# Performance work log

Hardware: AMD Instinct MI355X
Metric: run time of the kernel (lower is better)

Reference implementation:

```python
import jax, jax.numpy as jnp
import numpy as np

B, S, HID = 1, 2048, 2048
HQ, HKV, D = 16, 4, 128
BS = 64            # seerattn gate block size
GH = 128           # gate hidden size
INTER = 5632
THR = 0.004        # seerattn_threshold on softmaxed block gate scores
EPS = 1e-6
NEG = -1e30


def _rms(x, w):
    xf = x.astype(jnp.float32)
    var = jnp.mean(xf * xf, axis=-1, keepdims=True)
    return (w * (xf * jax.lax.rsqrt(var + EPS))).astype(x.dtype)


def _rotate_half(x):
    x1, x2 = jnp.split(x, 2, axis=-1)
    return jnp.concatenate([-x2, x1], axis=-1)


def setup_inputs() -> dict:
    key = jax.random.key(0)
    ks = jax.random.split(key, 16)
    s = 0.02
    pos = jnp.arange(S, dtype=jnp.float32)
    inv_freq = 1.0 / (1e6 ** (jnp.arange(0, D, 2, dtype=jnp.float32) / D))
    freqs = pos[:, None] * inv_freq[None, :]
    emb = jnp.concatenate([freqs, freqs], axis=-1)  # [S, D]
    return {
        'hidden_states': jax.random.normal(ks[0], (B, S, HID), jnp.float32),
        'cos': jnp.cos(emb),
        'sin': jnp.sin(emb),
        'ln1_w': jnp.ones((HID,), jnp.float32),
        'ln2_w': jnp.ones((HID,), jnp.float32),
        'Wq': jax.random.normal(ks[1], (HID, HQ * D), jnp.float32) * s,
        'bq': jnp.zeros((HQ * D,), jnp.float32),
        'Wk': jax.random.normal(ks[2], (HID, HKV * D), jnp.float32) * s,
        'bk': jnp.zeros((HKV * D,), jnp.float32),
        'Wv': jax.random.normal(ks[3], (HID, HKV * D), jnp.float32) * s,
        'bv': jnp.zeros((HKV * D,), jnp.float32),
        'Wo': jax.random.normal(ks[4], (HQ * D, HID), jnp.float32) * s,
        'gWq': jax.random.normal(ks[5], (D, GH), jnp.float32) * s,
        'gWk': jax.random.normal(ks[6], (D, GH), jnp.float32) * s,
        'Wgate': jax.random.normal(ks[7], (HID, INTER), jnp.float32) * s,
        'Wup': jax.random.normal(ks[8], (HID, INTER), jnp.float32) * s,
        'Wdown': jax.random.normal(ks[9], (INTER, HID), jnp.float32) * s,
    }


def reference(hidden_states, cos, sin, ln1_w, ln2_w, Wq, bq, Wk, bk, Wv, bv, Wo,
              gWq, gWk, Wgate, Wup, Wdown):
    B_, S_, _ = hidden_states.shape
    QB = S_ // BS
    grp = HQ // HKV

    h = _rms(hidden_states, ln1_w)
    q = (h @ Wq + bq).reshape(B_, S_, HQ, D)
    k = (h @ Wk + bk).reshape(B_, S_, HKV, D)
    v = (h @ Wv + bv).reshape(B_, S_, HKV, D)

    # ---- learned block gate (pre-RoPE q/k), threshold sparsity method ----
    qg = jnp.einsum('bshd,dg->bshg', q, gWq)
    qg = qg.reshape(B_, QB, BS, HQ, GH).mean(axis=2)            # [B, QB, HQ, GH]
    kp = k.reshape(B_, QB, BS, HKV, D).mean(axis=2)             # block-pooled K
    kg = jnp.einsum('bkhd,dg->bkhg', kp, gWk)
    kg = jnp.repeat(kg, grp, axis=2)                            # GQA -> HQ heads
    gscore = jnp.einsum('bqhg,bkhg->bhqk', qg, kg) * (GH ** -0.5)

    bidx = jnp.arange(QB)
    blk_causal = bidx[:, None] >= bidx[None, :]                 # [QB, QB]
    gscore = jnp.where(blk_causal[None, None], gscore, NEG)
    gate = jax.nn.softmax(gscore, axis=-1)                      # [B, HQ, QB, QB]

    diag = bidx[:, None] == bidx[None, :]
    keep = blk_causal[None, None] & ((gate >= THR) | diag[None, None])

    # ---- RoPE (unsqueeze_dim=2, layout [B,S,H,D]) ----
    c = cos[None, :, None, :]
    sn = sin[None, :, None, :]
    q = q * c + _rotate_half(q) * sn
    k = k * c + _rotate_half(k) * sn

    k = jnp.repeat(k, grp, axis=2)
    v = jnp.repeat(v, grp, axis=2)

    # ---- block-sparse masked attention (reference: dense w/ block mask) ----
    scores = jnp.einsum('bqhd,bkhd->bhqk', q, k) * (D ** -0.5)
    tok_keep = jnp.repeat(jnp.repeat(keep, BS, axis=2), BS, axis=3)
    tidx = jnp.arange(S_)
    tok_causal = tidx[:, None] >= tidx[None, :]
    mask = tok_keep & tok_causal[None, None]
    scores = jnp.where(mask, scores, NEG)
    p = jax.nn.softmax(scores, axis=-1)
    o = jnp.einsum('bhqk,bkhd->bqhd', p, v).reshape(B_, S_, HQ * D)
    attn_out = o @ Wo

    h2 = hidden_states + attn_out
    h3 = _rms(h2, ln2_w)
    mlp = (jax.nn.silu(h3 @ Wgate) * (h3 @ Wup)) @ Wdown
    return h2 + mlp
```

## Files before the change

### kernel.cpp

```cpp
#include <hip/hip_runtime.h>
#include <stdint.h>
#include <stddef.h>

#define S_LEN 2048
#define HIDN  2048
#define HQ    16
#define HKV   4
#define HDIM  128
#define NQKV  3072
#define QBLK  32
#define GHW   128
#define INTER 5632
#define NEGF  (-1e30f)
#define THRG  0.004f

typedef short bf16x8 __attribute__((ext_vector_type(8)));
typedef float f32x4  __attribute__((ext_vector_type(4)));

__device__ __forceinline__ short f2bf(float f) {
  union { float f; unsigned u; } v; v.f = f;
  unsigned r = (v.u + 0x7FFFu + ((v.u >> 16) & 1u)) >> 16;
  return (short)r;
}
__device__ __forceinline__ float bf2f(short s) {
  union { float f; unsigned u; } v; v.u = ((unsigned)(unsigned short)s) << 16;
  return v.f;
}
__device__ __forceinline__ void gload16(const void* g, void* l) {
  __builtin_amdgcn_global_load_lds(
      (const __attribute__((address_space(1))) void*)g,
      (__attribute__((address_space(3))) void*)l, 16, 0, 0);
}
__device__ __forceinline__ unsigned pack_bf2(float hi, float lo) {
  return __builtin_amdgcn_perm(__float_as_uint(hi), __float_as_uint(lo), 0x07060302u);
}

__global__ __launch_bounds__(256) void k_transpose_cast(
    const float* __restrict__ src, short* __restrict__ dst, int R, int C) {
  __shared__ float t[32][33];
  const int tx = threadIdx.x, ty = threadIdx.y;
  const int x = blockIdx.x * 32 + tx;
  const int y0 = blockIdx.y * 32;
#pragma unroll
  for (int i = 0; i < 4; i++) {
    int yy = ty + i * 8;
    t[yy][tx] = src[(long)(y0 + yy) * C + x];
  }
  __syncthreads();
  const int xo = blockIdx.y * 32 + tx;
  const int yo0 = blockIdx.x * 32;
#pragma unroll
  for (int i = 0; i < 4; i++) {
    int yy = ty + i * 8;
    dst[(long)(yo0 + yy) * R + xo] = f2bf(t[tx][yy]);
  }
}

__global__ void k_bias_concat(const float* __restrict__ bq, const float* __restrict__ bk,
                              const float* __restrict__ bv, float* __restrict__ out) {
  int i = blockIdx.x * 256 + threadIdx.x;
  if (i < 2048) out[i] = bq[i];
  else if (i < 2560) out[i] = bk[i - 2048];
  else out[i] = bv[i - 2560];
}

__global__ __launch_bounds__(256) void k_rms(const float* __restrict__ x,
                                             const float* __restrict__ w,
                                             short* __restrict__ out) {
  const int row = blockIdx.x;
  const float* xr = x + (long)row * HIDN;
  float v[8];
  float ss = 0.f;
#pragma unroll
  for (int i = 0; i < 8; i++) {
    v[i] = xr[threadIdx.x + i * 256];
    ss += v[i] * v[i];
  }
#pragma unroll
  for (int off = 32; off > 0; off >>= 1) ss += __shfl_down(ss, off, 64);
  __shared__ float red[4];
  const int wave = threadIdx.x >> 6, lane = threadIdx.x & 63;
  if (lane == 0) red[wave] = ss;
  __syncthreads();
  float tot = red[0] + red[1] + red[2] + red[3];
  float rs = rsqrtf(tot / (float)HIDN + 1e-6f);
#pragma unroll
  for (int i = 0; i < 8; i++) {
    int c = threadIdx.x + i * 256;
    out[(long)row * HIDN + c] = f2bf(v[i] * rs * w[c]);
  }
}

template <int MODE, int BN>
__global__ __launch_bounds__(256) void k_gemm(
    const short* __restrict__ A, const short* __restrict__ Bt,
    float* __restrict__ Cf, short* __restrict__ Cb,
    const float* __restrict__ bias, const float* __restrict__ add,
    const short* __restrict__ gaux, int M, int N, int K) {
  constexpr int NT = BN / 32;
  constexpr int BIW = BN / 32;
  constexpr int BPP = BN / 16;
  __shared__ short As[2][128][32];
  __shared__ short Bs[2][BN][32];
  const int tid = threadIdx.x;
  const int wave = tid >> 6, lane = tid & 63, quad = lane >> 4, l15 = lane & 15;
  const long m0 = (long)blockIdx.y * 128, n0 = (long)blockIdx.x * BN;
  const int wr = (wave >> 1) * 64, wc = (wave & 1) * (BN / 2);
  const int i2 = lane >> 2, i3 = lane & 3;
  f32x4 acc[4][NT] = {};
  const short* Ainst[4];
  short* Alds[4];
#pragma unroll
  for (int j = 0; j < 4; j++) {
    const int g = wave * 4 + j, h = g >> 3, rb = (g & 7) * 16;
    Ainst[j] = A + (m0 + rb + i2) * K + h * 32 + i3 * 8;
    Alds[j] = &As[h][rb][0];
  }
  const short* Binst[BIW];
  short* Blds[BIW];
#pragma unroll
  for (int j = 0; j < BIW; j++) {
    const int g = wave * BIW + j, h = g / BPP, rb = (g % BPP) * 16;
    Binst[j] = Bt + (n0 + rb + i2) * K + h * 32 + i3 * 8;
    Blds[j] = &Bs[h][rb][0];
  }
  for (int k0 = 0; k0 < K; k0 += 64) {
    __syncthreads();
#pragma unroll
    for (int j = 0; j < 4; j++) gload16(Ainst[j] + k0, Alds[j]);
#pragma unroll
    for (int j = 0; j < BIW; j++) gload16(Binst[j] + k0, Blds[j]);
    __syncthreads();
#pragma unroll
    for (int s = 0; s < 2; s++) {
      bf16x8 af[4], bb[NT];
#pragma unroll
      for (int mi = 0; mi < 4; mi++)
        af[mi] = *(const bf16x8*)&As[s][wr + mi * 16 + l15][quad * 8];
#pragma unroll
      for (int ni = 0; ni < NT; ni++)
        bb[ni] = *(const bf16x8*)&Bs[s][wc + ni * 16 + l15][quad * 8];
#pragma unroll
      for (int mi = 0; mi < 4; mi++)
#pragma unroll
        for (int ni = 0; ni < NT; ni++)
          acc[mi][ni] = __builtin_amdgcn_mfma_f32_16x16x32_bf16(af[mi], bb[ni], acc[mi][ni], 0, 0, 0);
    }
  }
  const bool hb = (MODE == 0) && (bias != nullptr);
  const bool ha = (MODE == 0) && (add != nullptr);
#pragma unroll
  for (int mi = 0; mi < 4; mi++) {
#pragma unroll
    for (int ni = 0; ni < NT; ni++) {
      long mbase = m0 + wr + mi * 16 + quad * 4;
      long n = n0 + wc + ni * 16 + l15;
#pragma unroll
      for (int r = 0; r < 4; r++) {
        float v = acc[mi][ni][r];
        long idx = (mbase + r) * N + n;
        if (MODE == 0) {
          if (hb) v += bias[n];
          if (ha) v += add[idx];
          Cf[idx] = v;
        } else if (MODE == 1) {
          Cb[idx] = f2bf(v);
        } else {
          float g = bf2f(gaux[idx]);
          float sg = g / (1.f + __expf(-g));
          Cb[idx] = f2bf(sg * v);
        }
      }
    }
  }
}

__global__ __launch_bounds__(256) void k_blockmean(const float* __restrict__ qkv,
                                                   float* __restrict__ qm,
                                                   float* __restrict__ km) {
  int id = blockIdx.x * 256 + threadIdx.x;
  int qb = id / 2560, c = id % 2560;
  const float* base = qkv + (long)qb * 64 * NQKV + c;
  float acc = 0.f;
  for (int s = 0; s < 64; s++) acc += base[(long)s * NQKV];
  acc *= (1.f / 64.f);
  if (c < 2048) qm[(long)qb * 2048 + c] = acc;
  else km[(long)qb * 512 + (c - 2048)] = acc;
}

__global__ __launch_bounds__(128) void k_gateproj(const float* __restrict__ qm,
                                                  const float* __restrict__ km,
                                                  const float* __restrict__ gWq,
                                                  const float* __restrict__ gWk,
                                                  float* __restrict__ qg,
                                                  float* __restrict__ kg) {
  __shared__ float xm[128];
  const int b = blockIdx.x;
  const float* src; const float* W; float* dst;
  if (b < 512) { src = qm + (long)b * 128; W = gWq; dst = qg + (long)b * 128; }
  else { int r = b - 512; src = km + (long)r * 128; W = gWk; dst = kg + (long)r * 128; }
  xm[threadIdx.x] = src[threadIdx.x];
  __syncthreads();
  float acc = 0.f;
  for (int d = 0; d < 128; d++) acc += xm[d] * W[d * GHW + threadIdx.x];
  dst[threadIdx.x] = acc;
}

__global__ __launch_bounds__(64) void k_gatemask(const float* __restrict__ qg,
                                                 const float* __restrict__ kg,
                                                 unsigned char* __restrict__ mask) {
  const int qb = blockIdx.x, h = blockIdx.y;
  __shared__ float qv[128];
  const int t = threadIdx.x;
  qv[t] = qg[((long)qb * 16 + h) * 128 + t];
  qv[t + 64] = qg[((long)qb * 16 + h) * 128 + t + 64];
  __syncthreads();
  const int kb = t;
  float s = NEGF;
  if (kb < 32 && kb <= qb) {
    const float* kr = kg + ((long)kb * 4 + (h >> 2)) * 128;
    float acc = 0.f;
    for (int d = 0; d < 128; d++) acc += qv[d] * kr[d];
    s = acc * 0.08838834764831845f;
  }
  float m = s;
#pragma unroll
  for (int off = 32; off > 0; off >>= 1) m = fmaxf(m, __shfl_xor(m, off, 64));
  float e = (kb < 32 && kb <= qb) ? __expf(s - m) : 0.f;
  float sum = e;
#pragma unroll
  for (int off = 32; off > 0; off >>= 1) sum += __shfl_xor(sum, off, 64);
  if (kb < 32) {
    float gate = e / sum;
    bool keep = (kb <= qb) && (gate >= THRG || kb == qb);
    mask[((long)h * 32 + qb) * 32 + kb] = keep ? 1 : 0;
  }
}

__global__ __launch_bounds__(256) void k_rope(const float* __restrict__ qkv,
                                              const float* __restrict__ cosb,
                                              const float* __restrict__ sinb,
                                              short* __restrict__ q_bf,
                                              short* __restrict__ k_bf) {
  long id = (long)blockIdx.x * 256 + threadIdx.x;
  int d = (int)(id & 63);
  long rest = id >> 6;
  int head = (int)(rest % 20);
  int s = (int)(rest / 20);
  const float c = cosb[(long)s * HDIM + d];
  const float sn = sinb[(long)s * HDIM + d];
  if (head < HQ) {
    const float* src = qkv + (long)s * NQKV + head * HDIM;
    float x1 = src[d], x2 = src[d + 64];
    short* dst = q_bf + ((long)head * S_LEN + s) * HDIM;
    dst[d] = f2bf(x1 * c - x2 * sn);
    dst[d + 64] = f2bf(x2 * c + x1 * sn);
  } else {
    int hk = head - HQ;
    const float* src = qkv + (long)s * NQKV + 2048 + hk * HDIM;
    float x1 = src[d], x2 = src[d + 64];
    short* dst = k_bf + ((long)hk * S_LEN + s) * HDIM;
    dst[d] = f2bf(x1 * c - x2 * sn);
    dst[d + 64] = f2bf(x2 * c + x1 * sn);
  }
}

__global__ __launch_bounds__(256) void k_vcast_t(const float* __restrict__ qkv,
                                                 short* __restrict__ v_t) {
  __shared__ float t[32][33];
  const int hk = blockIdx.z;
  const int tx = threadIdx.x, ty = threadIdx.y;
  const int d0 = blockIdx.x * 32;
  const int s0 = blockIdx.y * 32;
  const float* src = qkv + 2560 + (long)hk * HDIM;
#pragma unroll
  for (int i = 0; i < 4; i++) {
    int s = ty + i * 8;
    t[s][tx] = src[(long)(s0 + s) * NQKV + d0 + tx];
  }
  __syncthreads();
  short* dst = v_t + (long)hk * HDIM * S_LEN;
#pragma unroll
  for (int i = 0; i < 4; i++) {
    int d = ty + i * 8;
    dst[(long)(d0 + d) * S_LEN + s0 + tx] = f2bf(t[tx][d]);
  }
}

__global__ __launch_bounds__(256) void k_attn(const short* __restrict__ q_bf,
                                              const short* __restrict__ k_bf,
                                              const short* __restrict__ v_t,
                                              const unsigned char* __restrict__ mask,
                                              short* __restrict__ o_bf) {
  const int qb = blockIdx.x, h = blockIdx.y;
  const int tid = threadIdx.x, wave = tid >> 6, lane = tid & 63;
  const int quad = lane >> 4, l15 = lane & 15;
  __shared__ short Ks[4 * 64 * 32];
  __shared__ short Vs[2 * 128 * 32];
  __shared__ short Ps[4][16 * 72];
  short* Pw = Ps[wave];
  const int hk = h >> 2;
  const unsigned char* mptr = mask + ((long)h * 32 + qb) * 32;
  const float SCL = 0.08838834764831845f * 1.4426950408889634f;
  const int qrow_g = qb * 64 + wave * 16 + l15;

  bf16x8 bq[4];
  {
    const short* qrp = q_bf + ((long)h * S_LEN + qrow_g) * HDIM + quad * 8;
#pragma unroll
    for (int kd = 0; kd < 4; kd++) bq[kd] = *(const bf16x8*)(qrp + kd * 32);
  }

  const short* kh = k_bf + (long)hk * S_LEN * HDIM;
  const short* vh = v_t + (long)hk * HDIM * S_LEN;

  const int i2 = lane >> 2, i3 = lane & 3;
  int koff[4], voff[4];
  const int vp = wave >> 1, vhh = wave & 1;
#pragma unroll
  for (int inst = 0; inst < 4; inst++) {
    koff[inst] = (inst * 16 + i2) * HDIM + wave * 32 + i3 * 8;
    voff[inst] = (vhh * 64 + inst * 16 + i2) * S_LEN + vp * 32 + i3 * 8;
  }

  f32x4 accO[8] = {};
  float mrow = -3.0e38f, lrow = 0.f;

  for (int kb = 0; kb <= qb; kb++) {
    if (!mptr[kb]) continue;
    __syncthreads();
    {
      const int kg = kb * 64 * HDIM;
      const int vg = kb * 64;
#pragma unroll
      for (int inst = 0; inst < 4; inst++) {
        gload16(kh + kg + koff[inst], &Ks[wave * 2048 + inst * 512]);
        gload16(vh + vg + voff[inst], &Vs[vp * 4096 + (vhh * 64 + inst * 16) * 32]);
      }
    }
    __syncthreads();

    f32x4 sv[4];
#pragma unroll
    for (int nt = 0; nt < 4; nt++) {
      f32x4 t = {};
#pragma unroll
      for (int kd = 0; kd < 4; kd++) {
        bf16x8 ka = *(const bf16x8*)&Ks[kd * 2048 + (nt * 16 + l15) * 32 + quad * 8];
        t = __builtin_amdgcn_mfma_f32_16x16x32_bf16(ka, bq[kd], t, 0, 0, 0);
      }
      sv[nt] = t;
    }
    float lmx = -__builtin_inff();
    if (kb < qb) {
#pragma unroll
      for (int nt = 0; nt < 4; nt++)
#pragma unroll
        for (int r = 0; r < 4; r++) {
          sv[nt][r] *= SCL;
          lmx = fmaxf(lmx, sv[nt][r]);
        }
    } else {
#pragma unroll
      for (int nt = 0; nt < 4; nt++)
#pragma unroll
        for (int r = 0; r < 4; r++) {
          const int kcol = kb * 64 + nt * 16 + quad * 4 + r;
          sv[nt][r] = (kcol <= qrow_g) ? sv[nt][r] * SCL : -__builtin_inff();
          lmx = fmaxf(lmx, sv[nt][r]);
        }
    }
    lmx = fmaxf(lmx, __shfl_xor(lmx, 16, 64));
    lmx = fmaxf(lmx, __shfl_xor(lmx, 32, 64));
    const float mnew = fmaxf(mrow, lmx);
    const float alpha = __builtin_amdgcn_exp2f(mrow - mnew);
    mrow = mnew;
    float psum = 0.f;
#pragma unroll
    for (int nt = 0; nt < 4; nt++) {
#pragma unroll
      for (int r = 0; r < 4; r++) {
        float p = __builtin_amdgcn_exp2f(sv[nt][r] - mnew);
        sv[nt][r] = p;
        psum += p;
      }
      uint2 u;
      u.x = pack_bf2(sv[nt][1], sv[nt][0]);
      u.y = pack_bf2(sv[nt][3], sv[nt][2]);
      *(uint2*)&Pw[l15 * 72 + nt * 16 + quad * 4] = u;
    }
    psum += __shfl_xor(psum, 16, 64);
    psum += __shfl_xor(psum, 32, 64);
    lrow = lrow * alpha + psum;
    float al[4];
#pragma unroll
    for (int r = 0; r < 4; r++) al[r] = __shfl(alpha, quad * 4 + r, 64);
#pragma unroll
    for (int dt = 0; dt < 8; dt++)
#pragma unroll
      for (int r = 0; r < 4; r++) accO[dt][r] *= al[r];
    asm volatile("s_waitcnt lgkmcnt(0)" ::: "memory");
    bf16x8 pf[2];
#pragma unroll
    for (int ksb = 0; ksb < 2; ksb++)
      pf[ksb] = *(const bf16x8*)&Pw[l15 * 72 + ksb * 32 + quad * 8];
#pragma unroll
    for (int dt = 0; dt < 8; dt++) {
#pragma unroll
      for (int ksb = 0; ksb < 2; ksb++) {
        bf16x8 vf = *(const bf16x8*)&Vs[ksb * 4096 + (dt * 16 + l15) * 32 + quad * 8];
        accO[dt] = __builtin_amdgcn_mfma_f32_16x16x32_bf16(pf[ksb], vf, accO[dt], 0, 0, 0);
      }
    }
  }
  const float linv = 1.f / lrow;
  float li[4];
#pragma unroll
  for (int r = 0; r < 4; r++) li[r] = __shfl(linv, quad * 4 + r, 64);
#pragma unroll
  for (int r = 0; r < 4; r++) {
    const long srow = (long)qb * 64 + wave * 16 + quad * 4 + r;
#pragma unroll
    for (int dt = 0; dt < 8; dt++)
      o_bf[srow * HIDN + h * HDIM + dt * 16 + l15] = f2bf(accO[dt][r] * li[r]);
  }
}

static constexpr size_t SZ_WQKVT = (size_t)NQKV * HIDN * 2;
static constexpr size_t SZ_WOT = (size_t)HIDN * HIDN * 2;
static constexpr size_t SZ_WBIG = (size_t)INTER * HIDN * 2;
static constexpr size_t OFF_WQKVT = 0;
static constexpr size_t OFF_WOT = OFF_WQKVT + SZ_WQKVT;
static constexpr size_t OFF_WGATET = OFF_WOT + SZ_WOT;
static constexpr size_t OFF_WUPT = OFF_WGATET + SZ_WBIG;
static constexpr size_t OFF_WDOWNT = OFF_WUPT + SZ_WBIG;
static constexpr size_t OFF_BIAS = OFF_WDOWNT + SZ_WBIG;
static constexpr size_t OFF_MASK = OFF_BIAS + 3072 * 4 + 4096;
static constexpr size_t OFF_QM = OFF_MASK + 16 * 32 * 32 + 4096;
static constexpr size_t OFF_KM = OFF_QM + (size_t)32 * 16 * 128 * 4;
static constexpr size_t OFF_QG = OFF_KM + (size_t)32 * 4 * 128 * 4;
static constexpr size_t OFF_KG = OFF_QG + (size_t)32 * 16 * 128 * 4;
static constexpr size_t OFF_H2 = OFF_KG + (size_t)32 * 4 * 128 * 4;
static constexpr size_t OFF_H3 = OFF_H2 + (size_t)S_LEN * HIDN * 4;
static constexpr size_t OFF_REGA = OFF_H3 + (size_t)S_LEN * HIDN * 2;
static constexpr size_t RA_HBF = 0;
static constexpr size_t RA_QBF = RA_HBF + (size_t)S_LEN * HIDN * 2;
static constexpr size_t RA_KBF = RA_QBF + (size_t)HQ * S_LEN * HDIM * 2;
static constexpr size_t RA_VT = RA_KBF + (size_t)HKV * S_LEN * HDIM * 2;
static constexpr size_t RA_OBF = RA_VT + (size_t)HKV * HDIM * S_LEN * 2;
static constexpr size_t SZ_REGA = RA_OBF + (size_t)S_LEN * HIDN * 2;
static constexpr size_t OFF_REGB = OFF_REGA + SZ_REGA;
static constexpr size_t SZ_REGB = (size_t)S_LEN * NQKV * 4;
static constexpr size_t TOTAL_WS = OFF_REGB + SZ_REGB;

extern "C" void kernel_launch(void* const* d_in, const int* in_sizes, int n_in,
                              void* d_out, int out_size, void* d_ws, size_t ws_size,
                              hipStream_t stream) {
  const float* hidden = (const float*)d_in[0];
  const float* cosb = (const float*)d_in[1];
  const float* sinb = (const float*)d_in[2];
  const float* ln1 = (const float*)d_in[3];
  const float* ln2 = (const float*)d_in[4];
  const float* Wq = (const float*)d_in[5];
  const float* bq = (const float*)d_in[6];
  const float* Wk = (const float*)d_in[7];
  const float* bk = (const float*)d_in[8];
  const float* Wv = (const float*)d_in[9];
  const float* bv = (const float*)d_in[10];
  const float* Wo = (const float*)d_in[11];
  const float* gWq = (const float*)d_in[12];
  const float* gWk = (const float*)d_in[13];
  const float* Wgate = (const float*)d_in[14];
  const float* Wup = (const float*)d_in[15];
  const float* Wdown = (const float*)d_in[16];

  if (ws_size < TOTAL_WS) return;

  char* ws = (char*)d_ws;
  short* WqkvT = (short*)(ws + OFF_WQKVT);
  short* WoT = (short*)(ws + OFF_WOT);
  short* WgateT = (short*)(ws + OFF_WGATET);
  short* WupT = (short*)(ws + OFF_WUPT);
  short* WdownT = (short*)(ws + OFF_WDOWNT);
  float* biasqkv = (float*)(ws + OFF_BIAS);
  unsigned char* maskb = (unsigned char*)(ws + OFF_MASK);
  float* qm = (float*)(ws + OFF_QM);
  float* km = (float*)(ws + OFF_KM);
  float* qg = (float*)(ws + OFF_QG);
  float* kg = (float*)(ws + OFF_KG);
  float* h2 = (float*)(ws + OFF_H2);
  short* h3_bf = (short*)(ws + OFF_H3);
  short* h_bf = (short*)(ws + OFF_REGA + RA_HBF);
  short* q_bf = (short*)(ws + OFF_REGA + RA_QBF);
  short* k_bf = (short*)(ws + OFF_REGA + RA_KBF);
  short* v_t = (short*)(ws + OFF_REGA + RA_VT);
  short* o_bf = (short*)(ws + OFF_REGA + RA_OBF);
  short* act_bf = (short*)(ws + OFF_REGA);
  float* qkv_f = (float*)(ws + OFF_REGB);
  short* g_bf = (short*)(ws + OFF_REGB);
  float* outp = (float*)d_out;

  dim3 tb(32, 8);
  k_transpose_cast<<<dim3(64, 64), tb, 0, stream>>>(Wq, WqkvT, HIDN, 2048);
  k_transpose_cast<<<dim3(16, 64), tb, 0, stream>>>(Wk, WqkvT + (size_t)2048 * HIDN, HIDN, 512);
  k_transpose_cast<<<dim3(16, 64), tb, 0, stream>>>(Wv, WqkvT + (size_t)2560 * HIDN, HIDN, 512);
  k_transpose_cast<<<dim3(64, 64), tb, 0, stream>>>(Wo, WoT, HIDN, HIDN);
  k_transpose_cast<<<dim3(176, 64), tb, 0, stream>>>(Wgate, WgateT, HIDN, INTER);
  k_transpose_cast<<<dim3(176, 64), tb, 0, stream>>>(Wup, WupT, HIDN, INTER);
  k_transpose_cast<<<dim3(64, 176), tb, 0, stream>>>(Wdown, WdownT, INTER, HIDN);
  k_bias_concat<<<12, 256, 0, stream>>>(bq, bk, bv, biasqkv);

  k_rms<<<S_LEN, 256, 0, stream>>>(hidden, ln1, h_bf);
  k_gemm<0, 128><<<dim3(NQKV / 128, S_LEN / 128), 256, 0, stream>>>(
      h_bf, WqkvT, qkv_f, nullptr, biasqkv, nullptr, nullptr, S_LEN, NQKV, HIDN);
  k_blockmean<<<320, 256, 0, stream>>>(qkv_f, qm, km);
  k_gateproj<<<640, 128, 0, stream>>>(qm, km, gWq, gWk, qg, kg);
  k_gatemask<<<dim3(32, 16), 64, 0, stream>>>(qg, kg, maskb);
  k_rope<<<10240, 256, 0, stream>>>(qkv_f, cosb, sinb, q_bf, k_bf);
  k_vcast_t<<<dim3(4, 64, 4), tb, 0, stream>>>(qkv_f, v_t);
  k_attn<<<dim3(32, 16), 256, 0, stream>>>(q_bf, k_bf, v_t, maskb, o_bf);
  k_gemm<0, 128><<<dim3(HIDN / 128, S_LEN / 128), 256, 0, stream>>>(
      o_bf, WoT, h2, nullptr, nullptr, hidden, nullptr, S_LEN, HIDN, HIDN);
  k_rms<<<S_LEN, 256, 0, stream>>>(h2, ln2, h3_bf);
  k_gemm<1, 128><<<dim3(INTER / 128, 16), 256, 0, stream>>>(
      h3_bf, WgateT, nullptr, g_bf, nullptr, nullptr, nullptr, S_LEN, INTER, HIDN);
  k_gemm<2, 128><<<dim3(INTER / 128, 16), 256, 0, stream>>>(
      h3_bf, WupT, nullptr, act_bf, nullptr, nullptr, g_bf, S_LEN, INTER, HIDN);
  k_gemm<0, 128><<<dim3(HIDN / 128, S_LEN / 128), 256, 0, stream>>>(
      act_bf, WdownT, outp, nullptr, nullptr, h2, nullptr, S_LEN, HIDN, INTER);
  (void)in_sizes; (void)n_in; (void)out_size;
}
```

Measured before the change: 732.7 us.

## Fuse gate/up GEMMs, split-K down projection, and narrow N tiles for QKV/O

The gate and up projections become one kernel that shares the A tile and applies SiLU*up in the epilogue, so the intermediate gate tensor is never written out and h3 is read once instead of twice. The down projection is split over K into two partial buffers, which a separate finish kernel sums together with the residual, to get more blocks in flight. The QKV and O GEMMs use 64-wide N tiles so they launch more workgroups. The costs are an extra fp32 partial-buffer round trip and one more launch, plus higher register and LDS use in the fused kernel.

```diff
diff --git a/kernel.cpp b/kernel.cpp
--- a/kernel.cpp
+++ b/kernel.cpp
@@ -94,9 +94,9 @@
 template <int MODE, int BN>
 __global__ __launch_bounds__(256) void k_gemm(
     const short* __restrict__ A, const short* __restrict__ Bt,
-    float* __restrict__ Cf, short* __restrict__ Cb,
+    float* __restrict__ Cf, float* __restrict__ Cf2,
     const float* __restrict__ bias, const float* __restrict__ add,
-    const short* __restrict__ gaux, int M, int N, int K) {
+    int M, int N, int K, int ksl) {
   constexpr int NT = BN / 32;
   constexpr int BIW = BN / 32;
   constexpr int BPP = BN / 16;
@@ -124,7 +124,9 @@
     Binst[j] = Bt + (n0 + rb + i2) * K + h * 32 + i3 * 8;
     Blds[j] = &Bs[h][rb][0];
   }
-  for (int k0 = 0; k0 < K; k0 += 64) {
+  const int kbeg = blockIdx.z * ksl;
+  const int kend = kbeg + ksl;
+  for (int k0 = kbeg; k0 < kend; k0 += 64) {
     __syncthreads();
 #pragma unroll
     for (int j = 0; j < 4; j++) gload16(Ainst[j] + k0, Alds[j]);
@@ -149,6 +151,7 @@
   }
   const bool hb = (MODE == 0) && (bias != nullptr);
   const bool ha = (MODE == 0) && (add != nullptr);
+  float* dstp = (MODE == 4) ? ((blockIdx.z == 0) ? Cf : Cf2) : Cf;
 #pragma unroll
   for (int mi = 0; mi < 4; mi++) {
 #pragma unroll
@@ -163,15 +166,102 @@
           if (hb) v += bias[n];
           if (ha) v += add[idx];
           Cf[idx] = v;
-        } else if (MODE == 1) {
-          Cb[idx] = f2bf(v);
         } else {
-          float g = bf2f(gaux[idx]);
-          float sg = g / (1.f + __expf(-g));
-          Cb[idx] = f2bf(sg * v);
+          dstp[idx] = v;
         }
       }
     }
+  }
+}
+
+__global__ __launch_bounds__(256) void k_gemm_gu(
+    const short* __restrict__ A, const short* __restrict__ Bg,
+    const short* __restrict__ Bu, short* __restrict__ Cb,
+    int M, int N, int K) {
+  __shared__ short As[2][128][32];
+  __shared__ short Gs[2][128][32];
+  __shared__ short Us[2][128][32];
+  const int tid = threadIdx.x;
+  const int wave = tid >> 6, lane = tid & 63, quad = lane >> 4, l15 = lane & 15;
+  const long m0 = (long)blockIdx.y * 128, n0 = (long)blockIdx.x * 128;
+  const int wr = (wave >> 1) * 64, wc = (wave & 1) * 64;
+  const int i2 = lane >> 2, i3 = lane & 3;
+  const long uoff = (long)(Bu - Bg);
+  f32x4 accg[4][4] = {}, accu[4][4] = {};
+  const short* Ainst[4];
+  short* Alds[4];
+  const short* Ginst[4];
+  short* Glds[4];
+  short* Ulds[4];
+#pragma unroll
+  for (int j = 0; j < 4; j++) {
+    const int g = wave * 4 + j, h = g >> 3, rb = (g & 7) * 16;
+    Ainst[j] = A + (m0 + rb + i2) * K + h * 32 + i3 * 8;
+    Alds[j] = &As[h][rb][0];
+    Ginst[j] = Bg + (n0 + rb + i2) * K + h * 32 + i3 * 8;
+    Glds[j] = &Gs[h][rb][0];
+    Ulds[j] = &Us[h][rb][0];
+  }
+  for (int k0 = 0; k0 < K; k0 += 64) {
+    __syncthreads();
+#pragma unroll
+    for (int j = 0; j < 4; j++) {
+      gload16(Ainst[j] + k0, Alds[j]);
+      gload16(Ginst[j] + k0, Glds[j]);
+      gload16(Ginst[j] + k0 + uoff, Ulds[j]);
+    }
+    __syncthreads();
+#pragma unroll
+    for (int s = 0; s < 2; s++) {
+      bf16x8 af[4], bg[4], bu[4];
+#pragma unroll
+      for (int mi = 0; mi < 4; mi++)
+        af[mi] = *(const bf16x8*)&As[s][wr + mi * 16 + l15][quad * 8];
+#pragma unroll
+      for (int ni = 0; ni < 4; ni++) {
+        bg[ni] = *(const bf16x8*)&Gs[s][wc + ni * 16 + l15][quad * 8];
+        bu[ni] = *(const bf16x8*)&Us[s][wc + ni * 16 + l15][quad * 8];
+      }
+#pragma unroll
+      for (int mi = 0; mi < 4; mi++)
+#pragma unroll
+        for (int ni = 0; ni < 4; ni++) {
+          accg[mi][ni] = __builtin_amdgcn_mfma_f32_16x16x32_bf16(af[mi], bg[ni], accg[mi][ni], 0, 0, 0);
+          accu[mi][ni] = __builtin_amdgcn_mfma_f32_16x16x32_bf16(af[mi], bu[ni], accu[mi][ni], 0, 0, 0);
+        }
+    }
+  }
+#pragma unroll
+  for (int mi = 0; mi < 4; mi++) {
+#pragma unroll
+    for (int ni = 0; ni < 4; ni++) {
+      long mbase = m0 + wr + mi * 16 + quad * 4;
+      long n = n0 + wc + ni * 16 + l15;
+#pragma unroll
+      for (int r = 0; r < 4; r++) {
+        float g = accg[mi][ni][r];
+        float u = accu[mi][ni][r];
+        float sg = g / (1.f + __expf(-g));
+        Cb[(mbase + r) * N + n] = f2bf(sg * u);
+      }
+    }
+  }
+}
+
+__global__ __launch_bounds__(256) void k_finish(const float* __restrict__ p0,
+                                                const float* __restrict__ h2,
+                                                float* __restrict__ out) {
+  const long n = (long)S_LEN * HIDN;
+  for (long i = ((long)blockIdx.x * 256 + threadIdx.x) * 4; i < n;
+       i += (long)gridDim.x * 256 * 4) {
+    float4 a = *(const float4*)(out + i);
+    float4 b = *(const float4*)(p0 + i);
+    float4 c = *(const float4*)(h2 + i);
+    a.x += b.x + c.x;
+    a.y += b.y + c.y;
+    a.z += b.z + c.z;
+    a.w += b.w + c.w;
+    *(float4*)(out + i) = a;
   }
 }
 
@@ -497,7 +587,7 @@
   short* o_bf = (short*)(ws + OFF_REGA + RA_OBF);
   short* act_bf = (short*)(ws + OFF_REGA);
   float* qkv_f = (float*)(ws + OFF_REGB);
-  short* g_bf = (short*)(ws + OFF_REGB);
+  float* p0f = (float*)(ws + OFF_REGB);
   float* outp = (float*)d_out;
 
   dim3 tb(32, 8);
@@ -511,22 +601,21 @@
   k_bias_concat<<<12, 256, 0, stream>>>(bq, bk, bv, biasqkv);
 
   k_rms<<<S_LEN, 256, 0, stream>>>(hidden, ln1, h_bf);
-  k_gemm<0, 128><<<dim3(NQKV / 128, S_LEN / 128), 256, 0, stream>>>(
-      h_bf, WqkvT, qkv_f, nullptr, biasqkv, nullptr, nullptr, S_LEN, NQKV, HIDN);
+  k_gemm<0, 64><<<dim3(NQKV / 64, S_LEN / 128), 256, 0, stream>>>(
+      h_bf, WqkvT, qkv_f, nullptr, biasqkv, nullptr, S_LEN, NQKV, HIDN, HIDN);
   k_blockmean<<<320, 256, 0, stream>>>(qkv_f, qm, km);
   k_gateproj<<<640, 128, 0, stream>>>(qm, km, gWq, gWk, qg, kg);
   k_gatemask<<<dim3(32, 16), 64, 0, stream>>>(qg, kg, maskb);
   k_rope<<<10240, 256, 0, stream>>>(qkv_f, cosb, sinb, q_bf, k_bf);
   k_vcast_t<<<dim3(4, 64, 4), tb, 0, stream>>>(qkv_f, v_t);
   k_attn<<<dim3(32, 16), 256, 0, stream>>>(q_bf, k_bf, v_t, maskb, o_bf);
-  k_gemm<0, 128><<<dim3(HIDN / 128, S_LEN / 128), 256, 0, stream>>>(
-      o_bf, WoT, h2, nullptr, nullptr, hidden, nullptr, S_LEN, HIDN, HIDN);
+  k_gemm<0, 64><<<dim3(HIDN / 64, S_LEN / 128), 256, 0, stream>>>(
+      o_bf, WoT, h2, nullptr, nullptr, hidden, S_LEN, HIDN, HIDN, HIDN);
   k_rms<<<S_LEN, 256, 0, stream>>>(h2, ln2, h3_bf);
-  k_gemm<1, 128><<<dim3(INTER / 128, 16), 256, 0, stream>>>(
-      h3_bf, WgateT, nullptr, g_bf, nullptr, nullptr, nullptr, S_LEN, INTER, HIDN);
-  k_gemm<2, 128><<<dim3(INTER / 128, 16), 256, 0, stream>>>(
-      h3_bf, WupT, nullptr, act_bf, nullptr, nullptr, g_bf, S_LEN, INTER, HIDN);
-  k_gemm<0, 128><<<dim3(HIDN / 128, S_LEN / 128), 256, 0, stream>>>(
-      act_bf, WdownT, outp, nullptr, nullptr, h2, nullptr, S_LEN, HIDN, INTER);
+  k_gemm_gu<<<dim3(INTER / 128, S_LEN / 128), 256, 0, stream>>>(
+      h3_bf, WgateT, WupT, act_bf, S_LEN, INTER, HIDN);
+  k_gemm<4, 64><<<dim3(HIDN / 64, S_LEN / 128, 2), 256, 0, stream>>>(
+      act_bf, WdownT, p0f, outp, nullptr, nullptr, S_LEN, HIDN, INTER, INTER / 2);
+  k_finish<<<2048, 256, 0, stream>>>(p0f, h2, outp);
   (void)in_sizes; (void)n_in; (void)out_size;
 }
```

Result: faster. 699.8 us (-4.5%).

## Split-K the Wo and Wdown GEMMs with narrower tiles and fused residual epilogues

Applied to the files above, without the earlier changes.

The Wo and Wdown GEMMs now use 64-wide N tiles and split K in two. Each half writes partial sums to its own buffer. A new fused kernel adds the residual and computes RMSNorm after the Wo GEMM, and a final elementwise kernel sums the two Wdown partials with h2. The QKV GEMM also moves to 64-wide tiles. The aim is more workgroups on a 256-CU-class device for these N=2048 GEMMs, which otherwise launch only 256 blocks, at the cost of extra fp32 partial-sum traffic and one extra pass.

```diff
diff --git a/kernel.cpp b/kernel.cpp
--- a/kernel.cpp
+++ b/kernel.cpp
@@ -91,12 +91,44 @@
   }
 }
 
+__global__ __launch_bounds__(256) void k_rms_fin(const float* __restrict__ p0,
+                                                 const float* __restrict__ hid,
+                                                 const float* __restrict__ w,
+                                                 float* __restrict__ h2,
+                                                 short* __restrict__ out) {
+  const int row = blockIdx.x;
+  const long base = (long)row * HIDN;
+  float v[8];
+  float ss = 0.f;
+#pragma unroll
+  for (int i = 0; i < 8; i++) {
+    int c = threadIdx.x + i * 256;
+    float t = p0[base + c] + h2[base + c] + hid[base + c];
+    h2[base + c] = t;
+    v[i] = t;
+    ss += t * t;
+  }
+#pragma unroll
+  for (int off = 32; off > 0; off >>= 1) ss += __shfl_down(ss, off, 64);
+  __shared__ float red[4];
+  const int wave = threadIdx.x >> 6, lane = threadIdx.x & 63;
+  if (lane == 0) red[wave] = ss;
+  __syncthreads();
+  float tot = red[0] + red[1] + red[2] + red[3];
+  float rs = rsqrtf(tot / (float)HIDN + 1e-6f);
+#pragma unroll
+  for (int i = 0; i < 8; i++) {
+    int c = threadIdx.x + i * 256;
+    out[base + c] = f2bf(v[i] * rs * w[c]);
+  }
+}
+
 template <int MODE, int BN>
 __global__ __launch_bounds__(256) void k_gemm(
     const short* __restrict__ A, const short* __restrict__ Bt,
-    float* __restrict__ Cf, short* __restrict__ Cb,
+    float* __restrict__ Cf, float* __restrict__ Cf2, short* __restrict__ Cb,
     const float* __restrict__ bias, const float* __restrict__ add,
-    const short* __restrict__ gaux, int M, int N, int K) {
+    const short* __restrict__ gaux, int M, int N, int K, int ksl) {
   constexpr int NT = BN / 32;
   constexpr int BIW = BN / 32;
   constexpr int BPP = BN / 16;
@@ -124,7 +156,9 @@
     Binst[j] = Bt + (n0 + rb + i2) * K + h * 32 + i3 * 8;
     Blds[j] = &Bs[h][rb][0];
   }
-  for (int k0 = 0; k0 < K; k0 += 64) {
+  const int kbeg = (MODE == 4) ? blockIdx.z * ksl : 0;
+  const int kend = kbeg + ((MODE == 4) ? ksl : K);
+  for (int k0 = kbeg; k0 < kend; k0 += 64) {
     __syncthreads();
 #pragma unroll
     for (int j = 0; j < 4; j++) gload16(Ainst[j] + k0, Alds[j]);
@@ -149,6 +183,7 @@
   }
   const bool hb = (MODE == 0) && (bias != nullptr);
   const bool ha = (MODE == 0) && (add != nullptr);
+  float* dstp = (MODE == 4) ? ((blockIdx.z == 0) ? Cf : Cf2) : Cf;
 #pragma unroll
   for (int mi = 0; mi < 4; mi++) {
 #pragma unroll
@@ -165,13 +200,32 @@
           Cf[idx] = v;
         } else if (MODE == 1) {
           Cb[idx] = f2bf(v);
-        } else {
+        } else if (MODE == 2) {
           float g = bf2f(gaux[idx]);
           float sg = g / (1.f + __expf(-g));
           Cb[idx] = f2bf(sg * v);
+        } else {
+          dstp[idx] = v;
         }
       }
     }
+  }
+}
+
+__global__ __launch_bounds__(256) void k_finish(const float* __restrict__ p0,
+                                                const float* __restrict__ h2,
+                                                float* __restrict__ out) {
+  const long n = (long)S_LEN * HIDN;
+  for (long i = ((long)blockIdx.x * 256 + threadIdx.x) * 4; i < n;
+       i += (long)gridDim.x * 256 * 4) {
+    float4 a = *(const float4*)(out + i);
+    float4 b = *(const float4*)(p0 + i);
+    float4 c = *(const float4*)(h2 + i);
+    a.x += b.x + c.x;
+    a.y += b.y + c.y;
+    a.z += b.z + c.z;
+    a.w += b.w + c.w;
+    *(float4*)(out + i) = a;
   }
 }
 
@@ -497,6 +551,7 @@
   short* o_bf = (short*)(ws + OFF_REGA + RA_OBF);
   short* act_bf = (short*)(ws + OFF_REGA);
   float* qkv_f = (float*)(ws + OFF_REGB);
+  float* p0f = (float*)(ws + OFF_REGB);
   short* g_bf = (short*)(ws + OFF_REGB);
   float* outp = (float*)d_out;
 
@@ -511,22 +566,23 @@
   k_bias_concat<<<12, 256, 0, stream>>>(bq, bk, bv, biasqkv);
 
   k_rms<<<S_LEN, 256, 0, stream>>>(hidden, ln1, h_bf);
-  k_gemm<0, 128><<<dim3(NQKV / 128, S_LEN / 128), 256, 0, stream>>>(
-      h_bf, WqkvT, qkv_f, nullptr, biasqkv, nullptr, nullptr, S_LEN, NQKV, HIDN);
+  k_gemm<0, 64><<<dim3(NQKV / 64, S_LEN / 128), 256, 0, stream>>>(
+      h_bf, WqkvT, qkv_f, nullptr, nullptr, biasqkv, nullptr, nullptr, S_LEN, NQKV, HIDN, HIDN);
   k_blockmean<<<320, 256, 0, stream>>>(qkv_f, qm, km);
   k_gateproj<<<640, 128, 0, stream>>>(qm, km, gWq, gWk, qg, kg);
   k_gatemask<<<dim3(32, 16), 64, 0, stream>>>(qg, kg, maskb);
   k_rope<<<10240, 256, 0, stream>>>(qkv_f, cosb, sinb, q_bf, k_bf);
   k_vcast_t<<<dim3(4, 64, 4), tb, 0, stream>>>(qkv_f, v_t);
   k_attn<<<dim3(32, 16), 256, 0, stream>>>(q_bf, k_bf, v_t, maskb, o_bf);
-  k_gemm<0, 128><<<dim3(HIDN / 128, S_LEN / 128), 256, 0, stream>>>(
-      o_bf, WoT, h2, nullptr, nullptr, hidden, nullptr, S_LEN, HIDN, HIDN);
-  k_rms<<<S_LEN, 256, 0, stream>>>(h2, ln2, h3_bf);
-  k_gemm<1, 128><<<dim3(INTER / 128, 16), 256, 0, stream>>>(
-      h3_bf, WgateT, nullptr, g_bf, nullptr, nullptr, nullptr, S_LEN, INTER, HIDN);
-  k_gemm<2, 128><<<dim3(INTER / 128, 16), 256, 0, stream>>>(
-      h3_bf, WupT, nullptr, act_bf, nullptr, nullptr, g_bf, S_LEN, INTER, HIDN);
-  k_gemm<0, 128><<<dim3(HIDN / 128, S_LEN / 128), 256, 0, stream>>>(
-      act_bf, WdownT, outp, nullptr, nullptr, h2, nullptr, S_LEN, HIDN, INTER);
+  k_gemm<4, 64><<<dim3(HIDN / 64, S_LEN / 128, 2), 256, 0, stream>>>(
+      o_bf, WoT, p0f, h2, nullptr, nullptr, nullptr, nullptr, S_LEN, HIDN, HIDN, HIDN / 2);
+  k_rms_fin<<<S_LEN, 256, 0, stream>>>(p0f, hidden, ln2, h2, h3_bf);
+  k_gemm<1, 128><<<dim3(INTER / 128, S_LEN / 128), 256, 0, stream>>>(
+      h3_bf, WgateT, nullptr, nullptr, g_bf, nullptr, nullptr, nullptr, S_LEN, INTER, HIDN, HIDN);
+  k_gemm<2, 128><<<dim3(INTER / 128, S_LEN / 128), 256, 0, stream>>>(
+      h3_bf, WupT, nullptr, nullptr, act_bf, nullptr, nullptr, g_bf, S_LEN, INTER, HIDN, HIDN);
+  k_gemm<4, 64><<<dim3(HIDN / 64, S_LEN / 128, 2), 256, 0, stream>>>(
+      act_bf, WdownT, p0f, outp, nullptr, nullptr, nullptr, nullptr, S_LEN, HIDN, INTER, INTER / 2);
+  k_finish<<<2048, 256, 0, stream>>>(p0f, h2, outp);
   (void)in_sizes; (void)n_in; (void)out_size;
 }
```

Measured after the change: 656.7 us. 1.12x faster.
